# Performance work log

Measured on AMD Instinct MI355X. Metric: run time of the kernel, lower is better.

The kernel has to match this reference:

```python
import jax, jax.numpy as jnp
import numpy as np

E = 8          # n_experts
TOP_K = 2      # n_active_experts


def setup_inputs() -> dict:
    key = jax.random.key(0)
    ks = jax.random.split(key, 9)
    B, S, D, H = 4, 2048, 2048, 1408
    w = 0.02  # weight scale for numerical stability
    return {
        "x": jax.random.normal(ks[0], (B, S, D), dtype=jnp.float32),
        "gate_w": jax.random.normal(ks[1], (E, D), dtype=jnp.float32) * w,
        "expert_bias": jnp.zeros((E,), dtype=jnp.float32),
        "Wg": jax.random.normal(ks[2], (E, H, D), dtype=jnp.float32) * w,
        "Wu": jax.random.normal(ks[3], (E, H, D), dtype=jnp.float32) * w,
        "Wd": jax.random.normal(ks[4], (E, D, H), dtype=jnp.float32) * w,
        "Ws_g": jax.random.normal(ks[5], (H, D), dtype=jnp.float32) * w,
        "Ws_u": jax.random.normal(ks[6], (H, D), dtype=jnp.float32) * w,
        "Ws_d": jax.random.normal(ks[7], (D, H), dtype=jnp.float32) * w,
    }


def _swiglu(x, wg, wu, wd):
    # torch Linear layout: y = x @ W.T
    return (jax.nn.silu(x @ wg.T) * (x @ wu.T)) @ wd.T


def reference(x, gate_w, expert_bias, Wg, Wu, Wd, Ws_g, Ws_u, Ws_d):
    B, S, D = x.shape
    flat = x.reshape(-1, D)                      # [N, D]
    N = flat.shape[0]

    logits = flat @ gate_w.T                     # [N, E]
    probs = jax.nn.softmax(logits, axis=-1)
    biased = logits + expert_bias
    _, top_idx = jax.lax.top_k(biased, TOP_K)    # [N, K] (bias used only for selection)
    top_w = jnp.take_along_axis(probs, top_idx, axis=-1)
    top_w = top_w / jnp.sum(top_w, axis=-1, keepdims=True)

    # dense per-token combine weights: cw[n, e] = sum_k top_w[n,k] * (top_idx[n,k]==e)
    rows = jnp.arange(N)[:, None]
    cw = jnp.zeros((N, E), dtype=flat.dtype).at[rows, top_idx].add(top_w)

    out = jnp.zeros_like(flat)
    for e in range(E):  # fixed small expert count; equivalent to gather/scatter dispatch
        out = out + cw[:, e:e + 1] * _swiglu(flat, Wg[e], Wu[e], Wd[e])

    out = out + _swiglu(flat, Ws_g, Ws_u, Ws_d)  # shared expert
    return out.reshape(B, S, D)
```

## Files before the change

kernel.cpp:

```cpp
#include <hip/hip_runtime.h>
#include <hip/hip_bf16.h>

#define N_TOK 8192
#define DDIM  2048
#define HDIM  1408
#define ROWS_R 16384
#define ROWS_T 24576
#define MAXTILES 200

typedef unsigned short u16;
typedef unsigned int   u32;
typedef __bf16 bf16x8 __attribute__((ext_vector_type(8)));
typedef float  f32x4  __attribute__((ext_vector_type(4)));

__device__ __forceinline__ u16 f2bf(float f) {
  union { float f; u32 u; } v; v.f = f;
  u32 u = v.u;
  return (u16)((u + 0x7fffu + ((u >> 16) & 1u)) >> 16);
}
__device__ __forceinline__ float bf2f(u16 b) {
  union { u32 u; float f; } v; v.u = ((u32)b) << 16; return v.f;
}

typedef __attribute__((address_space(1))) void gvoid;
typedef __attribute__((address_space(3))) void lvoid;
__device__ __forceinline__ void gload16(const void* g, void* l) {
  __builtin_amdgcn_global_load_lds((gvoid*)g, (lvoid*)l, 16, 0, 0);
}

__global__ void k_gate(const float* __restrict__ x, const float* __restrict__ gw,
                       const float* __restrict__ bias, int* __restrict__ tok_idx,
                       float* __restrict__ wts, int* __restrict__ counts) {
  int lane = threadIdx.x & 63;
  int n = blockIdx.x * 4 + (threadIdx.x >> 6);
  const float* xr = x + (size_t)n * DDIM;
  float acc[8];
#pragma unroll
  for (int e = 0; e < 8; ++e) acc[e] = 0.f;
  for (int j = lane; j < DDIM; j += 64) {
    float xv = xr[j];
#pragma unroll
    for (int e = 0; e < 8; ++e) acc[e] += xv * gw[e * DDIM + j];
  }
#pragma unroll
  for (int e = 0; e < 8; ++e) {
#pragma unroll
    for (int off = 32; off > 0; off >>= 1) acc[e] += __shfl_xor(acc[e], off);
  }
  if (lane == 0) {
    float m = acc[0];
    for (int e = 1; e < 8; ++e) m = fmaxf(m, acc[e]);
    float p[8];
    for (int e = 0; e < 8; ++e) p[e] = expf(acc[e] - m);
    float b0[8];
    for (int e = 0; e < 8; ++e) b0[e] = acc[e] + bias[e];
    int i0 = 0;
    for (int e = 1; e < 8; ++e) if (b0[e] > b0[i0]) i0 = e;
    int i1 = (i0 == 0) ? 1 : 0;
    for (int e = 0; e < 8; ++e) if (e != i0 && b0[e] > b0[i1]) i1 = e;
    float w0 = p[i0], w1 = p[i1], inv = 1.f / (w0 + w1);
    tok_idx[2 * n] = i0; tok_idx[2 * n + 1] = i1;
    wts[2 * n] = w0 * inv; wts[2 * n + 1] = w1 * inv;
    atomicAdd(&counts[i0], 1); atomicAdd(&counts[i1], 1);
  }
}

__global__ void k_scan(const int* __restrict__ counts, int* __restrict__ offsets,
                       int* __restrict__ cursors, int* __restrict__ ntiles,
                       int4* __restrict__ tiles) {
  if (threadIdx.x != 0 || blockIdx.x != 0) return;
  int off = 0, idx = 0;
  for (int e = 0; e < 8; ++e) {
    offsets[e] = off; cursors[e] = 0;
    int T = counts[e];
    for (int r = 0; r < T; r += 128) {
      int nr = T - r; if (nr > 128) nr = 128;
      tiles[idx++] = make_int4(e, off + r, nr, 0);
    }
    off += T;
  }
  offsets[8] = off;
  for (int r = 0; r < N_TOK; r += 128)
    tiles[idx++] = make_int4(8, ROWS_R + r, 128, 0);
  *ntiles = idx;
}

__global__ void k_build(const int* __restrict__ tok_idx, const int* __restrict__ offsets,
                        int* __restrict__ cursors, int* __restrict__ token_ids,
                        int* __restrict__ pos) {
  int n = blockIdx.x * blockDim.x + threadIdx.x;
  if (n >= N_TOK) return;
#pragma unroll
  for (int s = 0; s < 2; ++s) {
    int e = tok_idx[2 * n + s];
    int p = offsets[e] + atomicAdd(&cursors[e], 1);
    token_ids[p] = n;
    pos[2 * n + s] = p;
  }
  token_ids[ROWS_R + n] = n;
}

__global__ void k_conv(const float* __restrict__ src, u16* __restrict__ dst, long n8) {
  long stride = (long)gridDim.x * blockDim.x;
  for (long i = (long)blockIdx.x * blockDim.x + threadIdx.x; i < n8; i += stride) {
    const float4* s = (const float4*)(src) + i * 2;
    float4 a = s[0], b = s[1];
    u32 p0 = (u32)f2bf(a.x) | ((u32)f2bf(a.y) << 16);
    u32 p1 = (u32)f2bf(a.z) | ((u32)f2bf(a.w) << 16);
    u32 p2 = (u32)f2bf(b.x) | ((u32)f2bf(b.y) << 16);
    u32 p3 = (u32)f2bf(b.z) | ((u32)f2bf(b.w) << 16);
    ((uint4*)dst)[i] = make_uint4(p0, p1, p2, p3);
  }
}

__global__ __launch_bounds__(256, 2) void k_gemm1(
    const u16* __restrict__ xb, const u16* __restrict__ wgb, const u16* __restrict__ wub,
    const int* __restrict__ token_ids, const int* __restrict__ ntiles,
    const int4* __restrict__ tiles, u16* __restrict__ h) {
  if ((int)blockIdx.y >= *ntiles) return;
  int4 tl = tiles[blockIdx.y];
  int set = tl.x, grow = tl.y, nrows = tl.z;
  int bx = blockIdx.x;
  __shared__ u16 As[128 * 64], Bgs[128 * 64], Bus[128 * 64];
  int t = threadIdx.x;
  int wid = t >> 6, lane = t & 63;

  const u16* aptr[4]; const u16* gptr[4]; const u16* uptr[4];
#pragma unroll
  for (int i = 0; i < 4; ++i) {
    int chunk = i * 256 + t;
    int r = chunk >> 3, cc = chunk & 7;
    int c = cc ^ (r & 7);
    int rr = r < nrows ? r : nrows - 1;
    int tok = token_ids[grow + rr];
    aptr[i] = xb + (size_t)tok * DDIM + c * 8;
    size_t wroff = (size_t)set * HDIM * DDIM + (size_t)(bx * 128 + r) * DDIM + c * 8;
    gptr[i] = wgb + wroff;
    uptr[i] = wub + wroff;
  }

  f32x4 accg[4][4], accu[4][4];
  f32x4 z = {0.f, 0.f, 0.f, 0.f};
#pragma unroll
  for (int m = 0; m < 4; ++m)
#pragma unroll
    for (int n = 0; n < 4; ++n) { accg[m][n] = z; accu[m][n] = z; }

  int wr = wid >> 1, wc = wid & 1;
  int l15 = lane & 15, lhi = lane >> 4;

  for (int k0 = 0; k0 < DDIM; k0 += 64) {
#pragma unroll
    for (int i = 0; i < 4; ++i) {
      int ldsoff = i * 4096 + wid * 1024;
      gload16(aptr[i] + k0, (char*)As + ldsoff);
      gload16(gptr[i] + k0, (char*)Bgs + ldsoff);
      gload16(uptr[i] + k0, (char*)Bus + ldsoff);
    }
    __syncthreads();
#pragma unroll
    for (int kk = 0; kk < 2; ++kk) {
      int cch = kk * 4 + lhi;
      bf16x8 af[4], bg[4], bu[4];
#pragma unroll
      for (int m = 0; m < 4; ++m) {
        int r = wr * 64 + m * 16 + l15;
        af[m] = *(const bf16x8*)((const char*)As + r * 128 + ((cch ^ (r & 7)) * 16));
      }
#pragma unroll
      for (int n = 0; n < 4; ++n) {
        int r = wc * 64 + n * 16 + l15;
        int boff = r * 128 + ((cch ^ (r & 7)) * 16);
        bg[n] = *(const bf16x8*)((const char*)Bgs + boff);
        bu[n] = *(const bf16x8*)((const char*)Bus + boff);
      }
#pragma unroll
      for (int m = 0; m < 4; ++m)
#pragma unroll
        for (int n = 0; n < 4; ++n) {
          accg[m][n] = __builtin_amdgcn_mfma_f32_16x16x32_bf16(af[m], bg[n], accg[m][n], 0, 0, 0);
          accu[m][n] = __builtin_amdgcn_mfma_f32_16x16x32_bf16(af[m], bu[n], accu[m][n], 0, 0, 0);
        }
    }
    __syncthreads();
  }

#pragma unroll
  for (int m = 0; m < 4; ++m) {
#pragma unroll
    for (int n = 0; n < 4; ++n) {
      int col = bx * 128 + wc * 64 + n * 16 + l15;
#pragma unroll
      for (int q = 0; q < 4; ++q) {
        int rl = wr * 64 + m * 16 + lhi * 4 + q;
        if (rl < nrows) {
          float g = accg[m][n][q], u = accu[m][n][q];
          float hv = g / (1.f + expf(-g)) * u;
          h[(size_t)(grow + rl) * HDIM + col] = f2bf(hv);
        }
      }
    }
  }
}

__global__ __launch_bounds__(256, 2) void k_gemm2(
    const u16* __restrict__ h, const u16* __restrict__ wdb,
    const int* __restrict__ ntiles, const int4* __restrict__ tiles,
    u16* __restrict__ y) {
  if ((int)blockIdx.y >= *ntiles) return;
  int4 tl = tiles[blockIdx.y];
  int set = tl.x, grow = tl.y, nrows = tl.z;
  int bx = blockIdx.x;
  __shared__ u16 As[128 * 64], Bs[128 * 64];
  int t = threadIdx.x, wid = t >> 6, lane = t & 63;

  const u16* aptr[4]; const u16* bptr[4];
#pragma unroll
  for (int i = 0; i < 4; ++i) {
    int chunk = i * 256 + t;
    int r = chunk >> 3, cc = chunk & 7;
    int c = cc ^ (r & 7);
    aptr[i] = h + (size_t)(grow + r) * HDIM + c * 8;
    bptr[i] = wdb + (size_t)set * DDIM * HDIM + (size_t)(bx * 128 + r) * HDIM + c * 8;
  }

  f32x4 acc[4][4];
  f32x4 z = {0.f, 0.f, 0.f, 0.f};
#pragma unroll
  for (int m = 0; m < 4; ++m)
#pragma unroll
    for (int n = 0; n < 4; ++n) acc[m][n] = z;

  int wr = wid >> 1, wc = wid & 1;
  int l15 = lane & 15, lhi = lane >> 4;

  for (int k0 = 0; k0 < HDIM; k0 += 64) {
#pragma unroll
    for (int i = 0; i < 4; ++i) {
      int ldsoff = i * 4096 + wid * 1024;
      gload16(aptr[i] + k0, (char*)As + ldsoff);
      gload16(bptr[i] + k0, (char*)Bs + ldsoff);
    }
    __syncthreads();
#pragma unroll
    for (int kk = 0; kk < 2; ++kk) {
      int cch = kk * 4 + lhi;
      bf16x8 af[4], bf[4];
#pragma unroll
      for (int m = 0; m < 4; ++m) {
        int r = wr * 64 + m * 16 + l15;
        af[m] = *(const bf16x8*)((const char*)As + r * 128 + ((cch ^ (r & 7)) * 16));
      }
#pragma unroll
      for (int n = 0; n < 4; ++n) {
        int r = wc * 64 + n * 16 + l15;
        bf[n] = *(const bf16x8*)((const char*)Bs + r * 128 + ((cch ^ (r & 7)) * 16));
      }
#pragma unroll
      for (int m = 0; m < 4; ++m)
#pragma unroll
        for (int n = 0; n < 4; ++n)
          acc[m][n] = __builtin_amdgcn_mfma_f32_16x16x32_bf16(af[m], bf[n], acc[m][n], 0, 0, 0);
    }
    __syncthreads();
  }

#pragma unroll
  for (int m = 0; m < 4; ++m) {
#pragma unroll
    for (int n = 0; n < 4; ++n) {
      int col = bx * 128 + wc * 64 + n * 16 + l15;
#pragma unroll
      for (int q = 0; q < 4; ++q) {
        int rl = wr * 64 + m * 16 + lhi * 4 + q;
        if (rl < nrows)
          y[(size_t)(grow + rl) * DDIM + col] = f2bf(acc[m][n][q]);
      }
    }
  }
}

__global__ void k_comb(const u16* __restrict__ y, const int* __restrict__ pos,
                       const float* __restrict__ wts, float* __restrict__ out) {
  int n = blockIdx.x;
  int c8 = threadIdx.x;
  int p0 = pos[2 * n], p1 = pos[2 * n + 1];
  float w0 = wts[2 * n], w1 = wts[2 * n + 1];
  uint4 a = ((const uint4*)(y + (size_t)p0 * DDIM))[c8];
  uint4 b = ((const uint4*)(y + (size_t)p1 * DDIM))[c8];
  uint4 c = ((const uint4*)(y + (size_t)(ROWS_R + n) * DDIM))[c8];
  float* o = out + (size_t)n * DDIM + c8 * 8;
#pragma unroll
  for (int j = 0; j < 4; ++j) {
    u32 ua = ((const u32*)&a)[j], ub = ((const u32*)&b)[j], uc = ((const u32*)&c)[j];
    o[2 * j]     = w0 * bf2f((u16)(ua & 0xffff)) + w1 * bf2f((u16)(ub & 0xffff)) + bf2f((u16)(uc & 0xffff));
    o[2 * j + 1] = w0 * bf2f((u16)(ua >> 16))    + w1 * bf2f((u16)(ub >> 16))    + bf2f((u16)(uc >> 16));
  }
}

extern "C" void kernel_launch(void* const* d_in, const int* in_sizes, int n_in,
                              void* d_out, int out_size, void* d_ws, size_t ws_size,
                              hipStream_t stream) {
  const float* x    = (const float*)d_in[0];
  const float* gw   = (const float*)d_in[1];
  const float* bias = (const float*)d_in[2];
  const float* Wg   = (const float*)d_in[3];
  const float* Wu   = (const float*)d_in[4];
  const float* Wd   = (const float*)d_in[5];
  const float* Wsg  = (const float*)d_in[6];
  const float* Wsu  = (const float*)d_in[7];
  const float* Wsd  = (const float*)d_in[8];
  float* out = (float*)d_out;

  char* ws = (char*)d_ws;
  size_t off = 0;
  auto alloc = [&](size_t bytes) -> void* {
    void* p = ws + off;
    off += (bytes + 255) & ~(size_t)255;
    return p;
  };
  u16* xb  = (u16*)alloc((size_t)N_TOK * DDIM * 2);
  u16* wgb = (u16*)alloc((size_t)9 * HDIM * DDIM * 2);
  u16* wub = (u16*)alloc((size_t)9 * HDIM * DDIM * 2);
  u16* wdb = (u16*)alloc((size_t)9 * DDIM * HDIM * 2);
  u16* h   = (u16*)alloc((size_t)ROWS_T * HDIM * 2);
  u16* y   = (u16*)alloc((size_t)ROWS_T * DDIM * 2);
  int*   token_ids = (int*)alloc(ROWS_T * 4);
  int*   tok_idx   = (int*)alloc(N_TOK * 2 * 4);
  int*   pos       = (int*)alloc(N_TOK * 2 * 4);
  float* wts       = (float*)alloc(N_TOK * 2 * 4);
  int*   counts  = (int*)alloc(8 * 4);
  int*   offsets = (int*)alloc(9 * 4);
  int*   cursors = (int*)alloc(8 * 4);
  int*   ntiles  = (int*)alloc(4);
  int4*  tiles   = (int4*)alloc(MAXTILES * 16);

  hipMemsetAsync(counts, 0, 8 * 4, stream);
  k_gate<<<N_TOK / 4, 256, 0, stream>>>(x, gw, bias, tok_idx, wts, counts);
  k_scan<<<1, 64, 0, stream>>>(counts, offsets, cursors, ntiles, tiles);
  k_build<<<(N_TOK + 255) / 256, 256, 0, stream>>>(tok_idx, offsets, cursors, token_ids, pos);

  k_conv<<<2048, 256, 0, stream>>>(x, xb, (long)N_TOK * DDIM / 8);
  k_conv<<<4096, 256, 0, stream>>>(Wg, wgb, (long)8 * HDIM * DDIM / 8);
  k_conv<<<512, 256, 0, stream>>>(Wsg, wgb + (size_t)8 * HDIM * DDIM, (long)HDIM * DDIM / 8);
  k_conv<<<4096, 256, 0, stream>>>(Wu, wub, (long)8 * HDIM * DDIM / 8);
  k_conv<<<512, 256, 0, stream>>>(Wsu, wub + (size_t)8 * HDIM * DDIM, (long)HDIM * DDIM / 8);
  k_conv<<<4096, 256, 0, stream>>>(Wd, wdb, (long)8 * DDIM * HDIM / 8);
  k_conv<<<512, 256, 0, stream>>>(Wsd, wdb + (size_t)8 * DDIM * HDIM, (long)DDIM * HDIM / 8);

  k_gemm1<<<dim3(HDIM / 128, MAXTILES), 256, 0, stream>>>(xb, wgb, wub, token_ids, ntiles, tiles, h);
  k_gemm2<<<dim3(DDIM / 128, MAXTILES), 256, 0, stream>>>(h, wdb, ntiles, tiles, y);
  k_comb<<<N_TOK, 256, 0, stream>>>(y, pos, wts, out);
}
```

Before: 942.4 us.

## Pipeline grouped GEMMs with 256-row tiles, LDS multi-buffering and XCD-aware scheduling

Both expert GEMMs move from 128x128 single-buffered tiles with full __syncthreads to 256x128 tiles on 512 threads, with double-buffered (gemm1) or triple-buffered (gemm2) LDS. Global-to-LDS loads are interleaved with MFMA quarters using explicit vmcnt/lgkmcnt waits, barriers and setprio. The launch becomes a 1D grid remapped so consecutive logical tiles stay on the same XCD. The x-to-bf16 conversion is fused into the gate kernel to drop one pass over x. Larger tiles waste more rows on partially filled expert tiles, and the hand-written waitcnt schedule is fragile.

```diff
diff --git a/kernel.cpp b/kernel.cpp
--- a/kernel.cpp
+++ b/kernel.cpp
@@ -6,7 +6,10 @@
 #define HDIM  1408
 #define ROWS_R 16384
 #define ROWS_T 24576
-#define MAXTILES 200
+#define MAXTILES 104
+#define BM 256
+#define BN 128
+#define BK 64
 
 typedef unsigned short u16;
 typedef unsigned int   u32;
@@ -28,19 +31,55 @@
   __builtin_amdgcn_global_load_lds((gvoid*)g, (lvoid*)l, 16, 0, 0);
 }
 
+#define BAR __builtin_amdgcn_s_barrier()
+#define SP1 __builtin_amdgcn_s_setprio(1)
+#define SP0 __builtin_amdgcn_s_setprio(0)
+#define LGK0 do { asm volatile("s_waitcnt lgkmcnt(0)" ::: "memory"); \
+                  __builtin_amdgcn_sched_barrier(0); } while (0)
+#define VMCNT(n) asm volatile("s_waitcnt vmcnt(" #n ")" ::: "memory")
+
+#define READ_AF(base, mb, dst) { \
+  _Pragma("unroll") for (int m_ = 0; m_ < 2; ++m_) { \
+    int r_ = wr * 64 + ((mb) + m_) * 16 + l15; \
+    _Pragma("unroll") for (int kk_ = 0; kk_ < 2; ++kk_) { \
+      int cch_ = kk_ * 4 + lhi; \
+      (dst)[m_ * 2 + kk_] = *(const bf16x8*)((const char*)(base) + r_ * 128 + ((cch_ ^ (r_ & 7)) * 16)); } } }
+
+#define READ_BF(base, dst) { \
+  _Pragma("unroll") for (int n_ = 0; n_ < 4; ++n_) { \
+    int r_ = wc * 64 + n_ * 16 + l15; \
+    _Pragma("unroll") for (int kk_ = 0; kk_ < 2; ++kk_) { \
+      int cch_ = kk_ * 4 + lhi; \
+      (dst)[n_ * 2 + kk_] = *(const bf16x8*)((const char*)(base) + r_ * 128 + ((cch_ ^ (r_ & 7)) * 16)); } } }
+
+#define MFMAQ(AF, BB, ACC, MB) { \
+  _Pragma("unroll") for (int m_ = 0; m_ < 2; ++m_) \
+  _Pragma("unroll") for (int n_ = 0; n_ < 4; ++n_) \
+  _Pragma("unroll") for (int kk_ = 0; kk_ < 2; ++kk_) \
+    (ACC)[(MB) + m_][n_] = __builtin_amdgcn_mfma_f32_16x16x32_bf16((AF)[m_ * 2 + kk_], (BB)[n_ * 2 + kk_], (ACC)[(MB) + m_][n_], 0, 0, 0); }
+
 __global__ void k_gate(const float* __restrict__ x, const float* __restrict__ gw,
                        const float* __restrict__ bias, int* __restrict__ tok_idx,
-                       float* __restrict__ wts, int* __restrict__ counts) {
+                       float* __restrict__ wts, int* __restrict__ counts,
+                       u16* __restrict__ xb) {
   int lane = threadIdx.x & 63;
   int n = blockIdx.x * 4 + (threadIdx.x >> 6);
   const float* xr = x + (size_t)n * DDIM;
+  u16* xbr = xb + (size_t)n * DDIM;
   float acc[8];
 #pragma unroll
   for (int e = 0; e < 8; ++e) acc[e] = 0.f;
-  for (int j = lane; j < DDIM; j += 64) {
-    float xv = xr[j];
-#pragma unroll
-    for (int e = 0; e < 8; ++e) acc[e] += xv * gw[e * DDIM + j];
+#pragma unroll 2
+  for (int j0 = 0; j0 < DDIM; j0 += 256) {
+    float4 xv = *(const float4*)(xr + j0 + lane * 4);
+    u32 p0 = (u32)f2bf(xv.x) | ((u32)f2bf(xv.y) << 16);
+    u32 p1 = (u32)f2bf(xv.z) | ((u32)f2bf(xv.w) << 16);
+    *(uint2*)(xbr + j0 + lane * 4) = make_uint2(p0, p1);
+#pragma unroll
+    for (int e = 0; e < 8; ++e) {
+      float4 gv = *(const float4*)(gw + e * DDIM + j0 + lane * 4);
+      acc[e] += xv.x * gv.x + xv.y * gv.y + xv.z * gv.z + xv.w * gv.w;
+    }
   }
 #pragma unroll
   for (int e = 0; e < 8; ++e) {
@@ -73,15 +112,15 @@
   for (int e = 0; e < 8; ++e) {
     offsets[e] = off; cursors[e] = 0;
     int T = counts[e];
-    for (int r = 0; r < T; r += 128) {
-      int nr = T - r; if (nr > 128) nr = 128;
+    for (int r = 0; r < T; r += BM) {
+      int nr = T - r; if (nr > BM) nr = BM;
       tiles[idx++] = make_int4(e, off + r, nr, 0);
     }
     off += T;
   }
   offsets[8] = off;
-  for (int r = 0; r < N_TOK; r += 128)
-    tiles[idx++] = make_int4(8, ROWS_R + r, 128, 0);
+  for (int r = 0; r < N_TOK; r += BM)
+    tiles[idx++] = make_int4(8, ROWS_R + r, BM, 0);
   *ntiles = idx;
 }
 
@@ -113,31 +152,59 @@
   }
 }
 
-__global__ __launch_bounds__(256, 2) void k_gemm1(
-    const u16* __restrict__ xb, const u16* __restrict__ wgb, const u16* __restrict__ wub,
+__global__ __launch_bounds__(512, 2) void k_gemm1(
+    const u16* __restrict__ xb, const u16* __restrict__ wgb,
     const int* __restrict__ token_ids, const int* __restrict__ ntiles,
     const int4* __restrict__ tiles, u16* __restrict__ h) {
-  if ((int)blockIdx.y >= *ntiles) return;
-  int4 tl = tiles[blockIdx.y];
+  __shared__ u16 As[2][BM * BK];
+  __shared__ u16 Bgs[2][BN * BK];
+  __shared__ u16 Bus[2][BN * BK];
+
+  int ntl = *ntiles;
+  int nwg = (HDIM / BN) * ntl;
+  int bid = blockIdx.x;
+  if (bid >= nwg) return;
+  int q8 = nwg >> 3, r8 = nwg & 7;
+  int xcd = bid & 7, pp = bid >> 3;
+  int lid = (xcd < r8 ? xcd * (q8 + 1) : r8 * (q8 + 1) + (xcd - r8) * q8) + pp;
+  int bx = lid / ntl, tile = lid - bx * ntl;
+
+  int4 tl = tiles[tile];
   int set = tl.x, grow = tl.y, nrows = tl.z;
-  int bx = blockIdx.x;
-  __shared__ u16 As[128 * 64], Bgs[128 * 64], Bus[128 * 64];
+
   int t = threadIdx.x;
   int wid = t >> 6, lane = t & 63;
-
-  const u16* aptr[4]; const u16* gptr[4]; const u16* uptr[4];
+  int wr = wid >> 1, wc = wid & 1;
+  int l15 = lane & 15, lhi = lane >> 4;
+
+  const u16* aptr[4];
 #pragma unroll
   for (int i = 0; i < 4; ++i) {
-    int chunk = i * 256 + t;
+    int chunk = i * 512 + t;
     int r = chunk >> 3, cc = chunk & 7;
     int c = cc ^ (r & 7);
     int rr = r < nrows ? r : nrows - 1;
     int tok = token_ids[grow + rr];
     aptr[i] = xb + (size_t)tok * DDIM + c * 8;
-    size_t wroff = (size_t)set * HDIM * DDIM + (size_t)(bx * 128 + r) * DDIM + c * 8;
-    gptr[i] = wgb + wroff;
-    uptr[i] = wub + wroff;
-  }
+  }
+  const u16* gptr[2];
+#pragma unroll
+  for (int i = 0; i < 2; ++i) {
+    int chunk = i * 512 + t;
+    int r = chunk >> 3, cc = chunk & 7;
+    int c = cc ^ (r & 7);
+    gptr[i] = wgb + (size_t)set * (HDIM * DDIM) + (size_t)(bx * BN + r) * DDIM + c * 8;
+  }
+  const size_t WUOFF = (size_t)9 * HDIM * DDIM;
+
+#define G1_A0(b, k0) { gload16(aptr[0] + (k0), (char*)As[b] + (size_t)t * 16); \
+                       gload16(aptr[1] + (k0), (char*)As[b] + (size_t)(512 + t) * 16); }
+#define G1_A1(b, k0) { gload16(aptr[2] + (k0), (char*)As[b] + (size_t)(1024 + t) * 16); \
+                       gload16(aptr[3] + (k0), (char*)As[b] + (size_t)(1536 + t) * 16); }
+#define G1_BG(b, k0) { gload16(gptr[0] + (k0), (char*)Bgs[b] + (size_t)t * 16); \
+                       gload16(gptr[1] + (k0), (char*)Bgs[b] + (size_t)(512 + t) * 16); }
+#define G1_BU(b, k0) { gload16(gptr[0] + WUOFF + (k0), (char*)Bus[b] + (size_t)t * 16); \
+                       gload16(gptr[1] + WUOFF + (k0), (char*)Bus[b] + (size_t)(512 + t) * 16); }
 
   f32x4 accg[4][4], accu[4][4];
   f32x4 z = {0.f, 0.f, 0.f, 0.f};
@@ -146,83 +213,119 @@
 #pragma unroll
     for (int n = 0; n < 4; ++n) { accg[m][n] = z; accu[m][n] = z; }
 
-  int wr = wid >> 1, wc = wid & 1;
-  int l15 = lane & 15, lhi = lane >> 4;
-
-  for (int k0 = 0; k0 < DDIM; k0 += 64) {
-#pragma unroll
-    for (int i = 0; i < 4; ++i) {
-      int ldsoff = i * 4096 + wid * 1024;
-      gload16(aptr[i] + k0, (char*)As + ldsoff);
-      gload16(gptr[i] + k0, (char*)Bgs + ldsoff);
-      gload16(uptr[i] + k0, (char*)Bus + ldsoff);
-    }
-    __syncthreads();
-#pragma unroll
-    for (int kk = 0; kk < 2; ++kk) {
-      int cch = kk * 4 + lhi;
-      bf16x8 af[4], bg[4], bu[4];
-#pragma unroll
-      for (int m = 0; m < 4; ++m) {
-        int r = wr * 64 + m * 16 + l15;
-        af[m] = *(const bf16x8*)((const char*)As + r * 128 + ((cch ^ (r & 7)) * 16));
-      }
-#pragma unroll
-      for (int n = 0; n < 4; ++n) {
-        int r = wc * 64 + n * 16 + l15;
-        int boff = r * 128 + ((cch ^ (r & 7)) * 16);
-        bg[n] = *(const bf16x8*)((const char*)Bgs + boff);
-        bu[n] = *(const bf16x8*)((const char*)Bus + boff);
-      }
-#pragma unroll
-      for (int m = 0; m < 4; ++m)
-#pragma unroll
-        for (int n = 0; n < 4; ++n) {
-          accg[m][n] = __builtin_amdgcn_mfma_f32_16x16x32_bf16(af[m], bg[n], accg[m][n], 0, 0, 0);
-          accu[m][n] = __builtin_amdgcn_mfma_f32_16x16x32_bf16(af[m], bu[n], accu[m][n], 0, 0, 0);
-        }
-    }
-    __syncthreads();
+  const int NK = DDIM / BK;
+
+  VMCNT(0);
+  G1_A0(0, 0); G1_A1(0, 0); G1_BG(0, 0); G1_BU(0, 0);
+  VMCNT(2); BAR;
+
+  for (int kt = 0; kt < NK - 1; ++kt) {
+    int cur = kt & 1, nxt = cur ^ 1;
+    int k1 = (kt + 1) * BK;
+    bf16x8 a01[4], a23[4], bb[8];
+    READ_AF(As[cur], 0, a01);
+    READ_BF(Bgs[cur], bb);
+    G1_A0(nxt, k1);
+    BAR; LGK0;
+    SP1; MFMAQ(a01, bb, accg, 0); SP0;
+    BAR;
+    READ_AF(As[cur], 2, a23);
+    G1_A1(nxt, k1);
+    BAR; LGK0;
+    SP1; MFMAQ(a23, bb, accg, 2); SP0;
+    VMCNT(4); BAR;
+    READ_BF(Bus[cur], bb);
+    G1_BG(nxt, k1);
+    BAR; LGK0;
+    SP1; MFMAQ(a01, bb, accu, 0); SP0;
+    BAR;
+    G1_BU(nxt, k1);
+    BAR;
+    SP1; MFMAQ(a23, bb, accu, 2); SP0;
+    VMCNT(2); BAR;
+  }
+  {
+    int cur = (NK - 1) & 1;
+    VMCNT(0); BAR;
+    bf16x8 a01[4], a23[4], bg8[8], bu8[8];
+    READ_AF(As[cur], 0, a01);
+    READ_AF(As[cur], 2, a23);
+    READ_BF(Bgs[cur], bg8);
+    READ_BF(Bus[cur], bu8);
+    LGK0;
+    MFMAQ(a01, bg8, accg, 0); MFMAQ(a23, bg8, accg, 2);
+    MFMAQ(a01, bu8, accu, 0); MFMAQ(a23, bu8, accu, 2);
   }
 
 #pragma unroll
   for (int m = 0; m < 4; ++m) {
 #pragma unroll
     for (int n = 0; n < 4; ++n) {
-      int col = bx * 128 + wc * 64 + n * 16 + l15;
-#pragma unroll
-      for (int q = 0; q < 4; ++q) {
-        int rl = wr * 64 + m * 16 + lhi * 4 + q;
+      int col = bx * BN + wc * 64 + n * 16 + l15;
+#pragma unroll
+      for (int qq = 0; qq < 4; ++qq) {
+        int rl = wr * 64 + m * 16 + lhi * 4 + qq;
         if (rl < nrows) {
-          float g = accg[m][n][q], u = accu[m][n][q];
+          float g = accg[m][n][qq], u = accu[m][n][qq];
           float hv = g / (1.f + expf(-g)) * u;
           h[(size_t)(grow + rl) * HDIM + col] = f2bf(hv);
         }
       }
     }
   }
-}
-
-__global__ __launch_bounds__(256, 2) void k_gemm2(
+#undef G1_A0
+#undef G1_A1
+#undef G1_BG
+#undef G1_BU
+}
+
+__global__ __launch_bounds__(512, 2) void k_gemm2(
     const u16* __restrict__ h, const u16* __restrict__ wdb,
     const int* __restrict__ ntiles, const int4* __restrict__ tiles,
     u16* __restrict__ y) {
-  if ((int)blockIdx.y >= *ntiles) return;
-  int4 tl = tiles[blockIdx.y];
+  __shared__ u16 As2[3][BM * BK];
+  __shared__ u16 Bs2[3][BN * BK];
+
+  int ntl = *ntiles;
+  int nwg = (DDIM / BN) * ntl;
+  int bid = blockIdx.x;
+  if (bid >= nwg) return;
+  int q8 = nwg >> 3, r8 = nwg & 7;
+  int xcd = bid & 7, pp = bid >> 3;
+  int lid = (xcd < r8 ? xcd * (q8 + 1) : r8 * (q8 + 1) + (xcd - r8) * q8) + pp;
+  int bx = lid / ntl, tile = lid - bx * ntl;
+
+  int4 tl = tiles[tile];
   int set = tl.x, grow = tl.y, nrows = tl.z;
-  int bx = blockIdx.x;
-  __shared__ u16 As[128 * 64], Bs[128 * 64];
-  int t = threadIdx.x, wid = t >> 6, lane = t & 63;
-
-  const u16* aptr[4]; const u16* bptr[4];
+
+  int t = threadIdx.x;
+  int wid = t >> 6, lane = t & 63;
+  int wr = wid >> 1, wc = wid & 1;
+  int l15 = lane & 15, lhi = lane >> 4;
+
+  const u16* aptr[4];
 #pragma unroll
   for (int i = 0; i < 4; ++i) {
-    int chunk = i * 256 + t;
+    int chunk = i * 512 + t;
     int r = chunk >> 3, cc = chunk & 7;
     int c = cc ^ (r & 7);
     aptr[i] = h + (size_t)(grow + r) * HDIM + c * 8;
-    bptr[i] = wdb + (size_t)set * DDIM * HDIM + (size_t)(bx * 128 + r) * HDIM + c * 8;
-  }
+  }
+  const u16* bptr[2];
+#pragma unroll
+  for (int i = 0; i < 2; ++i) {
+    int chunk = i * 512 + t;
+    int r = chunk >> 3, cc = chunk & 7;
+    int c = cc ^ (r & 7);
+    bptr[i] = wdb + (size_t)set * (DDIM * HDIM) + (size_t)(bx * BN + r) * HDIM + c * 8;
+  }
+
+#define G2_A(b, k0) { gload16(aptr[0] + (k0), (char*)As2[b] + (size_t)t * 16); \
+                      gload16(aptr[1] + (k0), (char*)As2[b] + (size_t)(512 + t) * 16); \
+                      gload16(aptr[2] + (k0), (char*)As2[b] + (size_t)(1024 + t) * 16); \
+                      gload16(aptr[3] + (k0), (char*)As2[b] + (size_t)(1536 + t) * 16); }
+#define G2_B(b, k0) { gload16(bptr[0] + (k0), (char*)Bs2[b] + (size_t)t * 16); \
+                      gload16(bptr[1] + (k0), (char*)Bs2[b] + (size_t)(512 + t) * 16); }
 
   f32x4 acc[4][4];
   f32x4 z = {0.f, 0.f, 0.f, 0.f};
@@ -231,53 +334,55 @@
 #pragma unroll
     for (int n = 0; n < 4; ++n) acc[m][n] = z;
 
-  int wr = wid >> 1, wc = wid & 1;
-  int l15 = lane & 15, lhi = lane >> 4;
-
-  for (int k0 = 0; k0 < HDIM; k0 += 64) {
-#pragma unroll
-    for (int i = 0; i < 4; ++i) {
-      int ldsoff = i * 4096 + wid * 1024;
-      gload16(aptr[i] + k0, (char*)As + ldsoff);
-      gload16(bptr[i] + k0, (char*)Bs + ldsoff);
-    }
-    __syncthreads();
-#pragma unroll
-    for (int kk = 0; kk < 2; ++kk) {
-      int cch = kk * 4 + lhi;
-      bf16x8 af[4], bf[4];
-#pragma unroll
-      for (int m = 0; m < 4; ++m) {
-        int r = wr * 64 + m * 16 + l15;
-        af[m] = *(const bf16x8*)((const char*)As + r * 128 + ((cch ^ (r & 7)) * 16));
-      }
-#pragma unroll
-      for (int n = 0; n < 4; ++n) {
-        int r = wc * 64 + n * 16 + l15;
-        bf[n] = *(const bf16x8*)((const char*)Bs + r * 128 + ((cch ^ (r & 7)) * 16));
-      }
-#pragma unroll
-      for (int m = 0; m < 4; ++m)
-#pragma unroll
-        for (int n = 0; n < 4; ++n)
-          acc[m][n] = __builtin_amdgcn_mfma_f32_16x16x32_bf16(af[m], bf[n], acc[m][n], 0, 0, 0);
-    }
-    __syncthreads();
+  const int NK2 = HDIM / BK;
+
+  VMCNT(0);
+  G2_A(0, 0); G2_B(0, 0);
+  G2_A(1, BK); G2_B(1, BK);
+  VMCNT(6); BAR;
+
+  for (int kt = 0; kt < NK2 - 2; ++kt) {
+    int cur = kt % 3, nx2 = (kt + 2) % 3;
+    int k2 = (kt + 2) * BK;
+    bf16x8 a01[4], a23[4], bb[8];
+    READ_AF(As2[cur], 0, a01);
+    READ_BF(Bs2[cur], bb);
+    G2_A(nx2, k2);
+    BAR; LGK0;
+    SP1; MFMAQ(a01, bb, acc, 0); SP0;
+    BAR;
+    READ_AF(As2[cur], 2, a23);
+    G2_B(nx2, k2);
+    BAR; LGK0;
+    SP1; MFMAQ(a23, bb, acc, 2); SP0;
+    VMCNT(6); BAR;
+  }
+  VMCNT(0); BAR;
+  for (int kt = NK2 - 2; kt < NK2; ++kt) {
+    int cur = kt % 3;
+    bf16x8 a01[4], a23[4], bb[8];
+    READ_AF(As2[cur], 0, a01);
+    READ_AF(As2[cur], 2, a23);
+    READ_BF(Bs2[cur], bb);
+    LGK0;
+    MFMAQ(a01, bb, acc, 0); MFMAQ(a23, bb, acc, 2);
   }
 
 #pragma unroll
   for (int m = 0; m < 4; ++m) {
 #pragma unroll
     for (int n = 0; n < 4; ++n) {
-      int col = bx * 128 + wc * 64 + n * 16 + l15;
-#pragma unroll
-      for (int q = 0; q < 4; ++q) {
-        int rl = wr * 64 + m * 16 + lhi * 4 + q;
+      int col = bx * BN + wc * 64 + n * 16 + l15;
+#pragma unroll
+      for (int qq = 0; qq < 4; ++qq) {
+        int rl = wr * 64 + m * 16 + lhi * 4 + qq;
         if (rl < nrows)
-          y[(size_t)(grow + rl) * DDIM + col] = f2bf(acc[m][n][q]);
+          y[(size_t)(grow + rl) * DDIM + col] = f2bf(acc[m][n][qq]);
       }
     }
   }
+#undef G2_A
+#undef G2_B
 }
 
 __global__ void k_comb(const u16* __restrict__ y, const int* __restrict__ pos,
@@ -336,11 +441,10 @@
   int4*  tiles   = (int4*)alloc(MAXTILES * 16);
 
   hipMemsetAsync(counts, 0, 8 * 4, stream);
-  k_gate<<<N_TOK / 4, 256, 0, stream>>>(x, gw, bias, tok_idx, wts, counts);
+  k_gate<<<N_TOK / 4, 256, 0, stream>>>(x, gw, bias, tok_idx, wts, counts, xb);
   k_scan<<<1, 64, 0, stream>>>(counts, offsets, cursors, ntiles, tiles);
   k_build<<<(N_TOK + 255) / 256, 256, 0, stream>>>(tok_idx, offsets, cursors, token_ids, pos);
 
-  k_conv<<<2048, 256, 0, stream>>>(x, xb, (long)N_TOK * DDIM / 8);
   k_conv<<<4096, 256, 0, stream>>>(Wg, wgb, (long)8 * HDIM * DDIM / 8);
   k_conv<<<512, 256, 0, stream>>>(Wsg, wgb + (size_t)8 * HDIM * DDIM, (long)HDIM * DDIM / 8);
   k_conv<<<4096, 256, 0, stream>>>(Wu, wub, (long)8 * HDIM * DDIM / 8);
@@ -348,7 +452,7 @@
   k_conv<<<4096, 256, 0, stream>>>(Wd, wdb, (long)8 * DDIM * HDIM / 8);
   k_conv<<<512, 256, 0, stream>>>(Wsd, wdb + (size_t)8 * DDIM * HDIM, (long)DDIM * HDIM / 8);
 
-  k_gemm1<<<dim3(HDIM / 128, MAXTILES), 256, 0, stream>>>(xb, wgb, wub, token_ids, ntiles, tiles, h);
-  k_gemm2<<<dim3(DDIM / 128, MAXTILES), 256, 0, stream>>>(h, wdb, ntiles, tiles, y);
+  k_gemm1<<<(HDIM / BN) * MAXTILES, 512, 0, stream>>>(xb, wgb, token_ids, ntiles, tiles, h);
+  k_gemm2<<<(DDIM / BN) * MAXTILES, 512, 0, stream>>>(h, wdb, ntiles, tiles, y);
   k_comb<<<N_TOK, 256, 0, stream>>>(y, pos, wts, out);
 }
```

Measured after the change: 935.8 us. No clear change (-0.7%).

## Fuse bf16 conversions into gate and GEMM loaders, add XCD-aware tile remap

Applied to the files above, without the earlier changes.

Removes the separate fp32→bf16 conversion kernels. Activations are now converted inside the gate kernel, and weights are converted on the fly inside the GEMM tile loaders with a packed cvt instruction before the LDS store. The GEMMs also switch to a 1D grid with an XCD-aware block remap so that consecutive tiles share L2. The cost moved is the standalone weight and activation conversion passes. In exchange the GEMMs read fp32 weights, twice the bytes, repeatedly across token tiles, and the weight load goes through registers instead of direct global-to-LDS loads.

```diff
diff --git a/kernel.cpp b/kernel.cpp
--- a/kernel.cpp
+++ b/kernel.cpp
@@ -7,6 +7,8 @@
 #define ROWS_R 16384
 #define ROWS_T 24576
 #define MAXTILES 200
+#define BM 128
+#define BK 64
 
 typedef unsigned short u16;
 typedef unsigned int   u32;
@@ -21,6 +23,11 @@
 __device__ __forceinline__ float bf2f(u16 b) {
   union { u32 u; float f; } v; v.u = ((u32)b) << 16; return v.f;
 }
+__device__ __forceinline__ u32 pkbf(float lo, float hi) {
+  u32 r;
+  asm volatile("v_cvt_pk_bf16_f32 %0, %1, %2" : "=v"(r) : "v"(lo), "v"(hi));
+  return r;
+}
 
 typedef __attribute__((address_space(1))) void gvoid;
 typedef __attribute__((address_space(3))) void lvoid;
@@ -30,17 +37,24 @@
 
 __global__ void k_gate(const float* __restrict__ x, const float* __restrict__ gw,
                        const float* __restrict__ bias, int* __restrict__ tok_idx,
-                       float* __restrict__ wts, int* __restrict__ counts) {
+                       float* __restrict__ wts, int* __restrict__ counts,
+                       u16* __restrict__ xb) {
   int lane = threadIdx.x & 63;
   int n = blockIdx.x * 4 + (threadIdx.x >> 6);
   const float* xr = x + (size_t)n * DDIM;
+  u16* xbr = xb + (size_t)n * DDIM;
   float acc[8];
 #pragma unroll
   for (int e = 0; e < 8; ++e) acc[e] = 0.f;
-  for (int j = lane; j < DDIM; j += 64) {
-    float xv = xr[j];
-#pragma unroll
-    for (int e = 0; e < 8; ++e) acc[e] += xv * gw[e * DDIM + j];
+#pragma unroll 2
+  for (int j0 = 0; j0 < DDIM; j0 += 256) {
+    float4 xv = *(const float4*)(xr + j0 + lane * 4);
+    *(uint2*)(xbr + j0 + lane * 4) = make_uint2(pkbf(xv.x, xv.y), pkbf(xv.z, xv.w));
+#pragma unroll
+    for (int e = 0; e < 8; ++e) {
+      float4 gv = *(const float4*)(gw + e * DDIM + j0 + lane * 4);
+      acc[e] += xv.x * gv.x + xv.y * gv.y + xv.z * gv.z + xv.w * gv.w;
+    }
   }
 #pragma unroll
   for (int e = 0; e < 8; ++e) {
@@ -73,15 +87,15 @@
   for (int e = 0; e < 8; ++e) {
     offsets[e] = off; cursors[e] = 0;
     int T = counts[e];
-    for (int r = 0; r < T; r += 128) {
-      int nr = T - r; if (nr > 128) nr = 128;
+    for (int r = 0; r < T; r += BM) {
+      int nr = T - r; if (nr > BM) nr = BM;
       tiles[idx++] = make_int4(e, off + r, nr, 0);
     }
     off += T;
   }
   offsets[8] = off;
-  for (int r = 0; r < N_TOK; r += 128)
-    tiles[idx++] = make_int4(8, ROWS_R + r, 128, 0);
+  for (int r = 0; r < N_TOK; r += BM)
+    tiles[idx++] = make_int4(8, ROWS_R + r, BM, 0);
   *ntiles = idx;
 }
 
@@ -100,32 +114,35 @@
   token_ids[ROWS_R + n] = n;
 }
 
-__global__ void k_conv(const float* __restrict__ src, u16* __restrict__ dst, long n8) {
-  long stride = (long)gridDim.x * blockDim.x;
-  for (long i = (long)blockIdx.x * blockDim.x + threadIdx.x; i < n8; i += stride) {
-    const float4* s = (const float4*)(src) + i * 2;
-    float4 a = s[0], b = s[1];
-    u32 p0 = (u32)f2bf(a.x) | ((u32)f2bf(a.y) << 16);
-    u32 p1 = (u32)f2bf(a.z) | ((u32)f2bf(a.w) << 16);
-    u32 p2 = (u32)f2bf(b.x) | ((u32)f2bf(b.y) << 16);
-    u32 p3 = (u32)f2bf(b.z) | ((u32)f2bf(b.w) << 16);
-    ((uint4*)dst)[i] = make_uint4(p0, p1, p2, p3);
-  }
-}
-
 __global__ __launch_bounds__(256, 2) void k_gemm1(
-    const u16* __restrict__ xb, const u16* __restrict__ wgb, const u16* __restrict__ wub,
+    const u16* __restrict__ xb,
+    const float* __restrict__ Wg, const float* __restrict__ Wsg,
+    const float* __restrict__ Wu, const float* __restrict__ Wsu,
     const int* __restrict__ token_ids, const int* __restrict__ ntiles,
     const int4* __restrict__ tiles, u16* __restrict__ h) {
-  if ((int)blockIdx.y >= *ntiles) return;
-  int4 tl = tiles[blockIdx.y];
+  __shared__ u16 As[128 * 64], Bgs[128 * 64], Bus[128 * 64];
+
+  int ntl = *ntiles;
+  const int NBX = HDIM / 128;
+  int nwg = NBX * ntl;
+  int bid = blockIdx.x;
+  if (bid >= nwg) return;
+  int q8 = nwg >> 3, r8 = nwg & 7;
+  int xcd = bid & 7, pp = bid >> 3;
+  int lid = (xcd < r8 ? xcd * (q8 + 1) : r8 * (q8 + 1) + (xcd - r8) * q8) + pp;
+  int tile = lid / NBX, bx = lid - tile * NBX;
+
+  int4 tl = tiles[tile];
   int set = tl.x, grow = tl.y, nrows = tl.z;
-  int bx = blockIdx.x;
-  __shared__ u16 As[128 * 64], Bgs[128 * 64], Bus[128 * 64];
+  const float* wgb = (set < 8) ? Wg + (size_t)set * HDIM * DDIM : Wsg;
+  const float* wub = (set < 8) ? Wu + (size_t)set * HDIM * DDIM : Wsu;
+
   int t = threadIdx.x;
   int wid = t >> 6, lane = t & 63;
-
-  const u16* aptr[4]; const u16* gptr[4]; const u16* uptr[4];
+  int wr = wid >> 1, wc = wid & 1;
+  int l15 = lane & 15, lhi = lane >> 4;
+
+  const u16* aptr[4]; const float* gptr[4]; const float* uptr[4];
 #pragma unroll
   for (int i = 0; i < 4; ++i) {
     int chunk = i * 256 + t;
@@ -134,7 +151,7 @@
     int rr = r < nrows ? r : nrows - 1;
     int tok = token_ids[grow + rr];
     aptr[i] = xb + (size_t)tok * DDIM + c * 8;
-    size_t wroff = (size_t)set * HDIM * DDIM + (size_t)(bx * 128 + r) * DDIM + c * 8;
+    size_t wroff = (size_t)(bx * 128 + r) * DDIM + c * 8;
     gptr[i] = wgb + wroff;
     uptr[i] = wub + wroff;
   }
@@ -146,16 +163,21 @@
 #pragma unroll
     for (int n = 0; n < 4; ++n) { accg[m][n] = z; accu[m][n] = z; }
 
-  int wr = wid >> 1, wc = wid & 1;
-  int l15 = lane & 15, lhi = lane >> 4;
-
-  for (int k0 = 0; k0 < DDIM; k0 += 64) {
+  for (int k0 = 0; k0 < DDIM; k0 += BK) {
+    __syncthreads();
+#pragma unroll
+    for (int i = 0; i < 4; ++i)
+      gload16(aptr[i] + k0, (char*)As + (size_t)(i * 256 + t) * 16);
 #pragma unroll
     for (int i = 0; i < 4; ++i) {
-      int ldsoff = i * 4096 + wid * 1024;
-      gload16(aptr[i] + k0, (char*)As + ldsoff);
-      gload16(gptr[i] + k0, (char*)Bgs + ldsoff);
-      gload16(uptr[i] + k0, (char*)Bus + ldsoff);
+      float4 g0 = *(const float4*)(gptr[i] + k0);
+      float4 g1 = *(const float4*)(gptr[i] + k0 + 4);
+      float4 u0 = *(const float4*)(uptr[i] + k0);
+      float4 u1 = *(const float4*)(uptr[i] + k0 + 4);
+      *(uint4*)((char*)Bgs + (size_t)(i * 256 + t) * 16) =
+          make_uint4(pkbf(g0.x, g0.y), pkbf(g0.z, g0.w), pkbf(g1.x, g1.y), pkbf(g1.z, g1.w));
+      *(uint4*)((char*)Bus + (size_t)(i * 256 + t) * 16) =
+          make_uint4(pkbf(u0.x, u0.y), pkbf(u0.z, u0.w), pkbf(u1.x, u1.y), pkbf(u1.z, u1.w));
     }
     __syncthreads();
 #pragma unroll
@@ -182,7 +204,6 @@
           accu[m][n] = __builtin_amdgcn_mfma_f32_16x16x32_bf16(af[m], bu[n], accu[m][n], 0, 0, 0);
         }
     }
-    __syncthreads();
   }
 
 #pragma unroll
@@ -191,10 +212,10 @@
     for (int n = 0; n < 4; ++n) {
       int col = bx * 128 + wc * 64 + n * 16 + l15;
 #pragma unroll
-      for (int q = 0; q < 4; ++q) {
-        int rl = wr * 64 + m * 16 + lhi * 4 + q;
+      for (int qq = 0; qq < 4; ++qq) {
+        int rl = wr * 64 + m * 16 + lhi * 4 + qq;
         if (rl < nrows) {
-          float g = accg[m][n][q], u = accu[m][n][q];
+          float g = accg[m][n][qq], u = accu[m][n][qq];
           float hv = g / (1.f + expf(-g)) * u;
           h[(size_t)(grow + rl) * HDIM + col] = f2bf(hv);
         }
@@ -204,24 +225,39 @@
 }
 
 __global__ __launch_bounds__(256, 2) void k_gemm2(
-    const u16* __restrict__ h, const u16* __restrict__ wdb,
+    const u16* __restrict__ h,
+    const float* __restrict__ Wd, const float* __restrict__ Wsd,
     const int* __restrict__ ntiles, const int4* __restrict__ tiles,
     u16* __restrict__ y) {
-  if ((int)blockIdx.y >= *ntiles) return;
-  int4 tl = tiles[blockIdx.y];
+  __shared__ u16 As[128 * 64], Bs[128 * 64];
+
+  int ntl = *ntiles;
+  const int NBX = DDIM / 128;
+  int nwg = NBX * ntl;
+  int bid = blockIdx.x;
+  if (bid >= nwg) return;
+  int q8 = nwg >> 3, r8 = nwg & 7;
+  int xcd = bid & 7, pp = bid >> 3;
+  int lid = (xcd < r8 ? xcd * (q8 + 1) : r8 * (q8 + 1) + (xcd - r8) * q8) + pp;
+  int tile = lid / NBX, bx = lid - tile * NBX;
+
+  int4 tl = tiles[tile];
   int set = tl.x, grow = tl.y, nrows = tl.z;
-  int bx = blockIdx.x;
-  __shared__ u16 As[128 * 64], Bs[128 * 64];
-  int t = threadIdx.x, wid = t >> 6, lane = t & 63;
-
-  const u16* aptr[4]; const u16* bptr[4];
+  const float* wdb = (set < 8) ? Wd + (size_t)set * DDIM * HDIM : Wsd;
+
+  int t = threadIdx.x;
+  int wid = t >> 6, lane = t & 63;
+  int wr = wid >> 1, wc = wid & 1;
+  int l15 = lane & 15, lhi = lane >> 4;
+
+  const u16* aptr[4]; const float* bptr[4];
 #pragma unroll
   for (int i = 0; i < 4; ++i) {
     int chunk = i * 256 + t;
     int r = chunk >> 3, cc = chunk & 7;
     int c = cc ^ (r & 7);
     aptr[i] = h + (size_t)(grow + r) * HDIM + c * 8;
-    bptr[i] = wdb + (size_t)set * DDIM * HDIM + (size_t)(bx * 128 + r) * HDIM + c * 8;
+    bptr[i] = wdb + (size_t)(bx * 128 + r) * HDIM + c * 8;
   }
 
   f32x4 acc[4][4];
@@ -231,15 +267,17 @@
 #pragma unroll
     for (int n = 0; n < 4; ++n) acc[m][n] = z;
 
-  int wr = wid >> 1, wc = wid & 1;
-  int l15 = lane & 15, lhi = lane >> 4;
-
-  for (int k0 = 0; k0 < HDIM; k0 += 64) {
+  for (int k0 = 0; k0 < HDIM; k0 += BK) {
+    __syncthreads();
+#pragma unroll
+    for (int i = 0; i < 4; ++i)
+      gload16(aptr[i] + k0, (char*)As + (size_t)(i * 256 + t) * 16);
 #pragma unroll
     for (int i = 0; i < 4; ++i) {
-      int ldsoff = i * 4096 + wid * 1024;
-      gload16(aptr[i] + k0, (char*)As + ldsoff);
-      gload16(bptr[i] + k0, (char*)Bs + ldsoff);
+      float4 b0 = *(const float4*)(bptr[i] + k0);
+      float4 b1 = *(const float4*)(bptr[i] + k0 + 4);
+      *(uint4*)((char*)Bs + (size_t)(i * 256 + t) * 16) =
+          make_uint4(pkbf(b0.x, b0.y), pkbf(b0.z, b0.w), pkbf(b1.x, b1.y), pkbf(b1.z, b1.w));
     }
     __syncthreads();
 #pragma unroll
@@ -262,7 +300,6 @@
         for (int n = 0; n < 4; ++n)
           acc[m][n] = __builtin_amdgcn_mfma_f32_16x16x32_bf16(af[m], bf[n], acc[m][n], 0, 0, 0);
     }
-    __syncthreads();
   }
 
 #pragma unroll
@@ -271,10 +308,10 @@
     for (int n = 0; n < 4; ++n) {
       int col = bx * 128 + wc * 64 + n * 16 + l15;
 #pragma unroll
-      for (int q = 0; q < 4; ++q) {
-        int rl = wr * 64 + m * 16 + lhi * 4 + q;
+      for (int qq = 0; qq < 4; ++qq) {
+        int rl = wr * 64 + m * 16 + lhi * 4 + qq;
         if (rl < nrows)
-          y[(size_t)(grow + rl) * DDIM + col] = f2bf(acc[m][n][q]);
+          y[(size_t)(grow + rl) * DDIM + col] = f2bf(acc[m][n][qq]);
       }
     }
   }
@@ -320,9 +357,6 @@
     return p;
   };
   u16* xb  = (u16*)alloc((size_t)N_TOK * DDIM * 2);
-  u16* wgb = (u16*)alloc((size_t)9 * HDIM * DDIM * 2);
-  u16* wub = (u16*)alloc((size_t)9 * HDIM * DDIM * 2);
-  u16* wdb = (u16*)alloc((size_t)9 * DDIM * HDIM * 2);
   u16* h   = (u16*)alloc((size_t)ROWS_T * HDIM * 2);
   u16* y   = (u16*)alloc((size_t)ROWS_T * DDIM * 2);
   int*   token_ids = (int*)alloc(ROWS_T * 4);
@@ -336,19 +370,12 @@
   int4*  tiles   = (int4*)alloc(MAXTILES * 16);
 
   hipMemsetAsync(counts, 0, 8 * 4, stream);
-  k_gate<<<N_TOK / 4, 256, 0, stream>>>(x, gw, bias, tok_idx, wts, counts);
+  k_gate<<<N_TOK / 4, 256, 0, stream>>>(x, gw, bias, tok_idx, wts, counts, xb);
   k_scan<<<1, 64, 0, stream>>>(counts, offsets, cursors, ntiles, tiles);
   k_build<<<(N_TOK + 255) / 256, 256, 0, stream>>>(tok_idx, offsets, cursors, token_ids, pos);
 
-  k_conv<<<2048, 256, 0, stream>>>(x, xb, (long)N_TOK * DDIM / 8);
-  k_conv<<<4096, 256, 0, stream>>>(Wg, wgb, (long)8 * HDIM * DDIM / 8);
-  k_conv<<<512, 256, 0, stream>>>(Wsg, wgb + (size_t)8 * HDIM * DDIM, (long)HDIM * DDIM / 8);
-  k_conv<<<4096, 256, 0, stream>>>(Wu, wub, (long)8 * HDIM * DDIM / 8);
-  k_conv<<<512, 256, 0, stream>>>(Wsu, wub + (size_t)8 * HDIM * DDIM, (long)HDIM * DDIM / 8);
-  k_conv<<<4096, 256, 0, stream>>>(Wd, wdb, (long)8 * DDIM * HDIM / 8);
-  k_conv<<<512, 256, 0, stream>>>(Wsd, wdb + (size_t)8 * DDIM * HDIM, (long)DDIM * HDIM / 8);
-
-  k_gemm1<<<dim3(HDIM / 128, MAXTILES), 256, 0, stream>>>(xb, wgb, wub, token_ids, ntiles, tiles, h);
-  k_gemm2<<<dim3(DDIM / 128, MAXTILES), 256, 0, stream>>>(h, wdb, ntiles, tiles, y);
+  k_gemm1<<<(HDIM / 128) * MAXTILES, 256, 0, stream>>>(xb, Wg, Wsg, Wu, Wsu,
+                                                       token_ids, ntiles, tiles, h);
+  k_gemm2<<<(DDIM / 128) * MAXTILES, 256, 0, stream>>>(h, Wd, Wsd, ntiles, tiles, y);
   k_comb<<<N_TOK, 256, 0, stream>>>(y, pos, wts, out);
 }
```

Result: slower. 1.076 ms (+14.2%).
